# Kernel optimization log

Hardware: AMD Instinct MI355X
Metric: run time of the kernel (lower is better)

Reference implementation:

```python
import jax, jax.numpy as jnp
import numpy as np

B, H, W, DIM = 4, 256, 256, 112
HEADS, DHEAD = 4, 28
WP = 478  # shifted mask width: 256 + 2*(DIM-1)


def _dwconv(x, w, b=None, pad=1):
    # x: [B,C,H,W], w: [C,1,kh,kw] depthwise
    C = x.shape[1]
    y = jax.lax.conv_general_dilated(
        x, w, (1, 1), [(pad, pad), (pad, pad)],
        dimension_numbers=('NCHW', 'OIHW', 'NCHW'),
        feature_group_count=C)
    if b is not None:
        y = y + b[None, :, None, None]
    return y


def _conv1x1(x, w, b):
    # x: [B,C,H,W], w: [O,C]
    return jnp.einsum('bchw,oc->bohw', x, w) + b[None, :, None, None]


def _shift_back(x, step=2):
    # x: [b,nC,row,col] -> [b,nC,row,row]; per-channel column shift by int(step*i)
    b, nC, row, col = x.shape
    ds = 256 // row
    s = float(step) / float(ds * ds)
    start = jnp.floor(jnp.arange(nC) * s).astype(jnp.int32)
    idx = start[:, None] + jnp.arange(row)  # [nC, out_col=row]
    return jnp.take_along_axis(x, idx[None, :, None, :], axis=3)


def setup_inputs() -> dict:
    key = jax.random.key(0)
    ks = jax.random.split(key, 16)
    s = 0.02
    f32 = jnp.float32
    return dict(
        x_in=jax.random.normal(ks[0], (B, H, W, DIM), f32),
        mask=jax.random.uniform(ks[1], (1, H, WP, DIM), f32),
        Wq=(jax.random.normal(ks[2], (DIM, DIM), f32) * s),
        Wk=(jax.random.normal(ks[3], (DIM, DIM), f32) * s),
        Wv=(jax.random.normal(ks[4], (DIM, DIM), f32) * s),
        rescale=jnp.ones((HEADS, 1, 1), f32),
        proj_w=(jax.random.normal(ks[5], (DIM, DIM), f32) * s),
        proj_b=jnp.zeros((DIM,), f32),
        pe_w1=(jax.random.normal(ks[6], (DIM, 1, 3, 3), f32) * s),
        pe_w2=(jax.random.normal(ks[7], (DIM, 1, 3, 3), f32) * s),
        mm_c1_w=(jax.random.normal(ks[8], (DIM, DIM), f32) * s),
        mm_c1_b=jnp.zeros((DIM,), f32),
        mm_c2_w=(jax.random.normal(ks[9], (DIM, DIM), f32) * s),
        mm_c2_b=jnp.zeros((DIM,), f32),
        mm_dw_w=(jax.random.normal(ks[10], (DIM, 1, 5, 5), f32) * s),
        mm_dw_b=jnp.zeros((DIM,), f32),
    )


def reference(x_in, mask, Wq, Wk, Wv, rescale, proj_w, proj_b, pe_w1, pe_w2,
              mm_c1_w, mm_c1_b, mm_c2_w, mm_c2_b, mm_dw_w, mm_dw_b):
    b, h, w, c = x_in.shape
    heads = rescale.shape[0]
    d = c // heads
    n = h * w
    x = x_in.reshape(b, n, c)
    q_inp = x @ Wq
    k_inp = x @ Wk
    v_inp = x @ Wv

    # MaskGuidedMechanism
    m = jnp.transpose(mask, (0, 3, 1, 2))  # [1,c,H,W']
    m1 = _conv1x1(m, mm_c1_w, mm_c1_b)
    amap = jax.nn.sigmoid(_dwconv(_conv1x1(m1, mm_c2_w, mm_c2_b), mm_dw_w, mm_dw_b, pad=2))
    ms = m1 * amap + m1
    mask_attn = jnp.transpose(_shift_back(ms), (0, 2, 3, 1))  # [1,h,w,c]
    mask_attn = jnp.broadcast_to(mask_attn, (b, h, w, c)).reshape(b, n, c)

    def split(t):  # [b,n,c] -> [b,heads,d,n]
        return t.reshape(b, n, heads, d).transpose(0, 2, 3, 1)

    q = split(q_inp)
    k = split(k_inp)
    v = split(v_inp * mask_attn)
    q = q / jnp.maximum(jnp.linalg.norm(q, axis=-1, keepdims=True), 1e-12)
    k = k / jnp.maximum(jnp.linalg.norm(k, axis=-1, keepdims=True), 1e-12)

    attn = jnp.einsum('bhdn,bhen->bhde', k, q) * rescale[None]  # [b,heads,d,d]
    attn = jax.nn.softmax(attn, axis=-1)
    xo = jnp.einsum('bhde,bhen->bhdn', attn, v)  # [b,heads,d,n]
    xo = xo.transpose(0, 3, 1, 2).reshape(b, n, heads * d)
    out_c = (xo @ proj_w + proj_b).reshape(b, h, w, c)

    vi = v_inp.reshape(b, h, w, c).transpose(0, 3, 1, 2)  # [b,c,h,w]
    pe = _dwconv(jax.nn.gelu(_dwconv(vi, pe_w1, None, pad=1), approximate=False), pe_w2, None, pad=1)
    return out_c + jnp.transpose(pe, (0, 2, 3, 1))
```

## Files before the change

### kernel.cpp

```cpp
#include <hip/hip_runtime.h>
#include <math.h>


#define NPX 262144
#define NB  65536
#define C   112
#define PM  122368
#define WPC 478

__global__ void k_transpose_w(const float* __restrict__ a, const float* __restrict__ b,
                              float* __restrict__ at, float* __restrict__ bt) {
    int i = blockIdx.x * 256 + threadIdx.x;
    if (i < C * C) {
        int o = i / C, c = i % C;
        at[c * C + o] = a[i];
        bt[c * C + o] = b[i];
    }
}

template <int MODE>
__global__ __launch_bounds__(256, 2) void k_gemm112(
    const float* __restrict__ in, const float* __restrict__ W,
    const float* __restrict__ bias, const float* __restrict__ mask,
    float* __restrict__ out) {
    __shared__ float xT[16 * 260];
    const int tid = threadIdx.x;
    const int lane = tid & 63;
    const int o0 = __builtin_amdgcn_readfirstlane(tid >> 6) * 28;
    const long px0 = (long)blockIdx.x * 256;
    const float* Wb = W;
    if (MODE == 1) Wb = W + (int)(px0 >> 16) * (C * C);

    float acc[4][28];
#pragma unroll
    for (int p = 0; p < 4; ++p)
#pragma unroll
        for (int j = 0; j < 28; ++j) acc[p][j] = 0.0f;

    for (int cc = 0; cc < C; cc += 16) {
        __syncthreads();
        {
            const int pxl = tid >> 2;
            const int cg = (tid & 3) * 4;
#pragma unroll
            for (int r = 0; r < 4; ++r) {
                const int p = pxl + r * 64;
                const long px = px0 + p;
                float4 v = *(const float4*)(in + px * C + cc + cg);
                if (MODE == 1) {
                    const float4 m = *(const float4*)(mask + (long)((int)(px & 65535)) * C + cc + cg);
                    v.x *= m.x; v.y *= m.y; v.z *= m.z; v.w *= m.w;
                }
                xT[(cg + 0) * 260 + p] = v.x;
                xT[(cg + 1) * 260 + p] = v.y;
                xT[(cg + 2) * 260 + p] = v.z;
                xT[(cg + 3) * 260 + p] = v.w;
            }
        }
        __syncthreads();
#pragma unroll
        for (int c = 0; c < 16; ++c) {
            const float4 a = *(const float4*)&xT[c * 260 + lane * 4];
            const float* wr = Wb + (cc + c) * C + o0;
            float wl[28];
#pragma unroll
            for (int j = 0; j < 28; ++j) wl[j] = wr[j];
#pragma unroll
            for (int j = 0; j < 28; ++j) {
                const float w = wl[j];
                acc[0][j] = fmaf(a.x, w, acc[0][j]);
                acc[1][j] = fmaf(a.y, w, acc[1][j]);
                acc[2][j] = fmaf(a.z, w, acc[2][j]);
                acc[3][j] = fmaf(a.w, w, acc[3][j]);
            }
        }
    }
    float bl[28];
#pragma unroll
    for (int j = 0; j < 28; ++j) bl[j] = bias ? bias[o0 + j] : 0.0f;
#pragma unroll
    for (int p = 0; p < 4; ++p) {
        const long px = px0 + (long)lane * 4 + p;
        float* dst = out + px * C + o0;
#pragma unroll
        for (int j4 = 0; j4 < 7; ++j4) {
            float4 vv;
            vv.x = acc[p][j4 * 4 + 0] + bl[j4 * 4 + 0];
            vv.y = acc[p][j4 * 4 + 1] + bl[j4 * 4 + 1];
            vv.z = acc[p][j4 * 4 + 2] + bl[j4 * 4 + 2];
            vv.w = acc[p][j4 * 4 + 3] + bl[j4 * 4 + 3];
            *(float4*)(dst + j4 * 4) = vv;
        }
    }
}

__global__ __launch_bounds__(256, 2) void k_syrk(const float* __restrict__ x,
                                                 float* __restrict__ part) {
    __shared__ float tile[16 * C];
    const int batch = blockIdx.x >> 7, seg = blockIdx.x & 127;
    const float* xb = x + ((long)batch * NB + (long)seg * 512) * C;
    const int ty = threadIdx.x >> 4, tx = threadIdx.x & 15;
    float acc[7][7];
#pragma unroll
    for (int i = 0; i < 7; ++i)
#pragma unroll
        for (int j = 0; j < 7; ++j) acc[i][j] = 0.0f;

    for (int ph = 0; ph < 32; ++ph) {
        __syncthreads();
        for (int i = threadIdx.x; i < 16 * C; i += 256)
            tile[i] = xb[ph * 16 * C + i];
        __syncthreads();
#pragma unroll 4
        for (int p = 0; p < 16; ++p) {
            float a[7], b[7];
#pragma unroll
            for (int i = 0; i < 7; ++i) a[i] = tile[p * C + ty * 7 + i];
#pragma unroll
            for (int j = 0; j < 7; ++j) b[j] = tile[p * C + tx * 7 + j];
#pragma unroll
            for (int i = 0; i < 7; ++i)
#pragma unroll
                for (int j = 0; j < 7; ++j)
                    acc[i][j] = fmaf(a[i], b[j], acc[i][j]);
        }
    }
    float* pb = part + (long)blockIdx.x * (C * C);
#pragma unroll
    for (int i = 0; i < 7; ++i)
#pragma unroll
        for (int j = 0; j < 7; ++j)
            pb[(ty * 7 + i) * C + tx * 7 + j] = acc[i][j];
}

__global__ void k_syrk_reduce(const float* __restrict__ part, float* __restrict__ S) {
    const int b = blockIdx.x;
    const int i = blockIdx.y * 256 + threadIdx.x;
    const float* p = part + (long)b * 128 * (C * C) + i;
    float s = 0.0f;
    for (int k = 0; k < 128; ++k) s += p[(long)k * (C * C)];
    S[b * (C * C) + i] = s;
}

__global__ void k_dw5(const float* __restrict__ m1, const float* __restrict__ t2,
                      const float* __restrict__ dww, const float* __restrict__ dwb,
                      float* __restrict__ ms) {
    const int px = blockIdx.x * 8 + (threadIdx.x >> 5);
    const int cs = threadIdx.x & 31;
    if (cs >= 28) return;
    const int c = cs * 4;
    const int r = px / WPC, w = px % WPC;
    float wv[4][25];
#pragma unroll
    for (int k = 0; k < 4; ++k)
#pragma unroll
        for (int t = 0; t < 25; ++t) wv[k][t] = dww[(c + k) * 25 + t];
    float a0 = dwb[c], a1 = dwb[c + 1], a2 = dwb[c + 2], a3 = dwb[c + 3];
#pragma unroll
    for (int ky = 0; ky < 5; ++ky) {
        const int rr = r + ky - 2;
        if (rr < 0 || rr > 255) continue;
#pragma unroll
        for (int kx = 0; kx < 5; ++kx) {
            const int ww = w + kx - 2;
            if (ww < 0 || ww > WPC - 1) continue;
            const float4 t = *(const float4*)&t2[(long)(rr * WPC + ww) * C + c];
            const int ki = ky * 5 + kx;
            a0 = fmaf(t.x, wv[0][ki], a0);
            a1 = fmaf(t.y, wv[1][ki], a1);
            a2 = fmaf(t.z, wv[2][ki], a2);
            a3 = fmaf(t.w, wv[3][ki], a3);
        }
    }
    a0 = 1.0f / (1.0f + expf(-a0));
    a1 = 1.0f / (1.0f + expf(-a1));
    a2 = 1.0f / (1.0f + expf(-a2));
    a3 = 1.0f / (1.0f + expf(-a3));
    const float4 m = *(const float4*)&m1[(long)px * C + c];
    ms[(long)(c + 0) * PM + px] = m.x * (1.0f + a0);
    ms[(long)(c + 1) * PM + px] = m.y * (1.0f + a1);
    ms[(long)(c + 2) * PM + px] = m.z * (1.0f + a2);
    ms[(long)(c + 3) * PM + px] = m.w * (1.0f + a3);
}

__global__ void k_gather(const float* __restrict__ ms, float* __restrict__ mattn) {
    __shared__ float t[64][116];
    const int r = blockIdx.x >> 2;
    const int col0 = (blockIdx.x & 3) * 64;
    for (int i = threadIdx.x; i < C * 64; i += 256) {
        const int c = i >> 6, j = i & 63;
        t[j][c] = ms[(long)c * PM + r * WPC + col0 + 2 * c + j];
    }
    __syncthreads();
    for (int i = threadIdx.x; i < 64 * C; i += 256) {
        const int j = i / C, c = i % C;
        mattn[(long)(r * 256 + col0 + j) * C + c] = t[j][c];
    }
}

__global__ void k_T12(const float* __restrict__ S, const float* __restrict__ Wq,
                      const float* __restrict__ Wk, float* __restrict__ T1, float* __restrict__ T2) {
    const int b = blockIdx.x, which = blockIdx.y;
    const float* Sb = S + b * (C * C);
    const float* W = which ? Wk : Wq;
    float* T = (which ? T2 : T1) + b * (C * C);
    const int i0 = blockIdx.z * 1792;
    for (int i = i0 + threadIdx.x; i < i0 + 1792; i += 256) {
        const int row = i / C, col = i % C;
        float s = 0.0f;
        for (int m = 0; m < C; ++m) s = fmaf(Sb[row * C + m], W[m * C + col], s);
        T[i] = s;
    }
}

__global__ void k_attn(const float* __restrict__ T1, const float* __restrict__ T2,
                       const float* __restrict__ Wq, const float* __restrict__ Wk,
                       const float* __restrict__ rescale, const float* __restrict__ proj_w,
                       float* __restrict__ Mb) {
    __shared__ float att[28][29];
    __shared__ float nk[28], nq[28];
    const int b = blockIdx.x >> 2, h = blockIdx.x & 3;
    const float* T1b = T1 + b * (C * C);
    const float* T2b = T2 + b * (C * C);
    const int base = h * 28;
    const int tid = threadIdx.x;
    if (tid < 28) {
        const int i = base + tid;
        float s = 0.0f;
        for (int m = 0; m < C; ++m) s = fmaf(Wq[m * C + i], T1b[m * C + i], s);
        nq[tid] = fmaxf(sqrtf(fmaxf(s, 0.0f)), 1e-12f);
    } else if (tid >= 32 && tid < 60) {
        const int e = tid - 32, i = base + e;
        float s = 0.0f;
        for (int m = 0; m < C; ++m) s = fmaf(Wk[m * C + i], T2b[m * C + i], s);
        nk[e] = fmaxf(sqrtf(fmaxf(s, 0.0f)), 1e-12f);
    }
    __syncthreads();
    const float rs = rescale[h];
    for (int i = tid; i < 784; i += 256) {
        const int d = i / 28, e = i % 28;
        float s = 0.0f;
        for (int m = 0; m < C; ++m) s = fmaf(Wk[m * C + base + d], T1b[m * C + base + e], s);
        att[d][e] = s / (nk[d] * nq[e]) * rs;
    }
    __syncthreads();
    if (tid < 28) {
        float mx = -1e30f;
        for (int e = 0; e < 28; ++e) mx = fmaxf(mx, att[tid][e]);
        float sum = 0.0f;
        for (int e = 0; e < 28; ++e) { const float ex = expf(att[tid][e] - mx); att[tid][e] = ex; sum += ex; }
        const float inv = 1.0f / sum;
        for (int e = 0; e < 28; ++e) att[tid][e] *= inv;
    }
    __syncthreads();
    for (int i = tid; i < 28 * C; i += 256) {
        const int e = i / C, o = i % C;
        float s = 0.0f;
        for (int d = 0; d < 28; ++d) s = fmaf(att[d][e], proj_w[(base + d) * C + o], s);
        Mb[b * (C * C) + (base + e) * C + o] = s;
    }
}

__global__ void k_pe1(const float* __restrict__ v, const float* __restrict__ w1, float* __restrict__ g) {
    const long px = (long)blockIdx.x * 8 + (threadIdx.x >> 5);
    const int cs = threadIdx.x & 31;
    if (cs >= 28) return;
    const int c = cs * 4;
    const int within = (int)(px & 65535);
    const long bb = px - within;
    const int r = within >> 8, w = within & 255;
    float wv[4][9];
#pragma unroll
    for (int k = 0; k < 4; ++k)
#pragma unroll
        for (int t = 0; t < 9; ++t) wv[k][t] = w1[(c + k) * 9 + t];
    float a0 = 0, a1 = 0, a2 = 0, a3 = 0;
#pragma unroll
    for (int ky = 0; ky < 3; ++ky) {
        const int rr = r + ky - 1;
        if (rr < 0 || rr > 255) continue;
#pragma unroll
        for (int kx = 0; kx < 3; ++kx) {
            const int ww = w + kx - 1;
            if (ww < 0 || ww > 255) continue;
            const float4 t = *(const float4*)&v[(bb + (rr << 8) + ww) * C + c];
            const int ki = ky * 3 + kx;
            a0 = fmaf(t.x, wv[0][ki], a0);
            a1 = fmaf(t.y, wv[1][ki], a1);
            a2 = fmaf(t.z, wv[2][ki], a2);
            a3 = fmaf(t.w, wv[3][ki], a3);
        }
    }
    a0 = 0.5f * a0 * (1.0f + erff(a0 * 0.70710678118654752f));
    a1 = 0.5f * a1 * (1.0f + erff(a1 * 0.70710678118654752f));
    a2 = 0.5f * a2 * (1.0f + erff(a2 * 0.70710678118654752f));
    a3 = 0.5f * a3 * (1.0f + erff(a3 * 0.70710678118654752f));
    *(float4*)&g[px * C + c] = make_float4(a0, a1, a2, a3);
}

__global__ void k_pe2(const float* __restrict__ g, const float* __restrict__ w2, float* __restrict__ out) {
    const long px = (long)blockIdx.x * 8 + (threadIdx.x >> 5);
    const int cs = threadIdx.x & 31;
    if (cs >= 28) return;
    const int c = cs * 4;
    const int within = (int)(px & 65535);
    const long bb = px - within;
    const int r = within >> 8, w = within & 255;
    float wv[4][9];
#pragma unroll
    for (int k = 0; k < 4; ++k)
#pragma unroll
        for (int t = 0; t < 9; ++t) wv[k][t] = w2[(c + k) * 9 + t];
    float a0 = 0, a1 = 0, a2 = 0, a3 = 0;
#pragma unroll
    for (int ky = 0; ky < 3; ++ky) {
        const int rr = r + ky - 1;
        if (rr < 0 || rr > 255) continue;
#pragma unroll
        for (int kx = 0; kx < 3; ++kx) {
            const int ww = w + kx - 1;
            if (ww < 0 || ww > 255) continue;
            const float4 t = *(const float4*)&g[(bb + (rr << 8) + ww) * C + c];
            const int ki = ky * 3 + kx;
            a0 = fmaf(t.x, wv[0][ki], a0);
            a1 = fmaf(t.y, wv[1][ki], a1);
            a2 = fmaf(t.z, wv[2][ki], a2);
            a3 = fmaf(t.w, wv[3][ki], a3);
        }
    }
    float4 o = *(const float4*)&out[px * C + c];
    o.x += a0; o.y += a1; o.z += a2; o.w += a3;
    *(float4*)&out[px * C + c] = o;
}

extern "C" void kernel_launch(void* const* d_in, const int* in_sizes, int n_in,
                              void* d_out, int out_size, void* d_ws, size_t ws_size,
                              hipStream_t stream) {
    const float* x_in    = (const float*)d_in[0];
    const float* maskp   = (const float*)d_in[1];
    const float* Wq      = (const float*)d_in[2];
    const float* Wk      = (const float*)d_in[3];
    const float* Wv      = (const float*)d_in[4];
    const float* rescale = (const float*)d_in[5];
    const float* proj_w  = (const float*)d_in[6];
    const float* proj_b  = (const float*)d_in[7];
    const float* pe_w1   = (const float*)d_in[8];
    const float* pe_w2   = (const float*)d_in[9];
    const float* c1w     = (const float*)d_in[10];
    const float* c1b     = (const float*)d_in[11];
    const float* c2w     = (const float*)d_in[12];
    const float* c2b     = (const float*)d_in[13];
    const float* dww     = (const float*)d_in[14];
    const float* dwb     = (const float*)d_in[15];

    float* ws    = (float*)d_ws;
    float* v_inp = ws;
    float* mbuf  = ws + 29360128;
    float* m1    = mbuf;
    float* t2    = mbuf + 13705216;
    float* ms    = mbuf + 27410432;
    float* g     = mbuf;
    float* mattn = ws + 70475776;
    float* part  = mattn;
    float* S     = ws + 77815808;
    float* T1    = ws + 77865984;
    float* T2    = ws + 77916160;
    float* Mb    = ws + 77966336;
    float* c1wT  = ws + 78016512;
    float* c2wT  = ws + 78029056;

    k_transpose_w<<<49, 256, 0, stream>>>(c1w, c2w, c1wT, c2wT);
    k_gemm112<0><<<1024, 256, 0, stream>>>(x_in, Wv, nullptr, nullptr, v_inp);
    k_syrk<<<512, 256, 0, stream>>>(x_in, part);
    k_syrk_reduce<<<dim3(4, 49), 256, 0, stream>>>(part, S);
    k_gemm112<0><<<478, 256, 0, stream>>>(maskp, c1wT, c1b, nullptr, m1);
    k_gemm112<0><<<478, 256, 0, stream>>>(m1, c2wT, c2b, nullptr, t2);
    k_dw5<<<15296, 256, 0, stream>>>(m1, t2, dww, dwb, ms);
    k_gather<<<1024, 256, 0, stream>>>(ms, mattn);
    k_T12<<<dim3(4, 2, 7), 256, 0, stream>>>(S, Wq, Wk, T1, T2);
    k_attn<<<16, 256, 0, stream>>>(T1, T2, Wq, Wk, rescale, proj_w, Mb);
    k_pe1<<<32768, 256, 0, stream>>>(v_inp, pe_w1, g);
    k_gemm112<1><<<1024, 256, 0, stream>>>(v_inp, Mb, proj_b, mattn, (float*)d_out);
    k_pe2<<<32768, 256, 0, stream>>>(g, pe_w2, (float*)d_out);
    (void)in_sizes; (void)n_in; (void)out_size; (void)ws_size;
}
```

Baseline: 1.203 ms.

## Register-tile depthwise convs over 4 pixels and rewrite SYRK without LDS

New measurement: 1.081 ms. -10.1%, faster.

```diff
diff --git a/kernel.cpp b/kernel.cpp
--- a/kernel.cpp
+++ b/kernel.cpp
@@ -9,12 +9,25 @@
 #define WPC 478
 
 __global__ void k_transpose_w(const float* __restrict__ a, const float* __restrict__ b,
-                              float* __restrict__ at, float* __restrict__ bt) {
-    int i = blockIdx.x * 256 + threadIdx.x;
+                              const float* __restrict__ dw, const float* __restrict__ p1,
+                              const float* __restrict__ p2,
+                              float* __restrict__ at, float* __restrict__ bt,
+                              float* __restrict__ dwt, float* __restrict__ p1t,
+                              float* __restrict__ p2t) {
+    const int i = blockIdx.x * 256 + threadIdx.x;
     if (i < C * C) {
-        int o = i / C, c = i % C;
-        at[c * C + o] = a[i];
-        bt[c * C + o] = b[i];
+        const int o = i / C, cc = i % C;
+        at[cc * C + o] = a[i];
+        bt[cc * C + o] = b[i];
+    }
+    if (i < 25 * C) {
+        const int t = i / C, ch = i % C;
+        dwt[i] = dw[ch * 25 + t];
+    }
+    if (i < 9 * C) {
+        const int t = i / C, ch = i % C;
+        p1t[i] = p1[ch * 9 + t];
+        p2t[i] = p2[ch * 9 + t];
     }
 }
 
@@ -94,43 +107,44 @@
     }
 }
 
-__global__ __launch_bounds__(256, 2) void k_syrk(const float* __restrict__ x,
-                                                 float* __restrict__ part) {
-    __shared__ float tile[16 * C];
-    const int batch = blockIdx.x >> 7, seg = blockIdx.x & 127;
-    const float* xb = x + ((long)batch * NB + (long)seg * 512) * C;
-    const int ty = threadIdx.x >> 4, tx = threadIdx.x & 15;
-    float acc[7][7];
-#pragma unroll
-    for (int i = 0; i < 7; ++i)
-#pragma unroll
-        for (int j = 0; j < 7; ++j) acc[i][j] = 0.0f;
-
-    for (int ph = 0; ph < 32; ++ph) {
-        __syncthreads();
-        for (int i = threadIdx.x; i < 16 * C; i += 256)
-            tile[i] = xb[ph * 16 * C + i];
-        __syncthreads();
-#pragma unroll 4
-        for (int p = 0; p < 16; ++p) {
-            float a[7], b[7];
-#pragma unroll
-            for (int i = 0; i < 7; ++i) a[i] = tile[p * C + ty * 7 + i];
-#pragma unroll
-            for (int j = 0; j < 7; ++j) b[j] = tile[p * C + tx * 7 + j];
-#pragma unroll
-            for (int i = 0; i < 7; ++i)
-#pragma unroll
-                for (int j = 0; j < 7; ++j)
-                    acc[i][j] = fmaf(a[i], b[j], acc[i][j]);
-        }
-    }
-    float* pb = part + (long)blockIdx.x * (C * C);
-#pragma unroll
-    for (int i = 0; i < 7; ++i)
-#pragma unroll
-        for (int j = 0; j < 7; ++j)
-            pb[(ty * 7 + i) * C + tx * 7 + j] = acc[i][j];
+__global__ __launch_bounds__(256) void k_syrk(const float* __restrict__ x,
+                                              float* __restrict__ part) {
+    const int blk = blockIdx.x;
+    const int batch = blk >> 7, seg = blk & 127;
+    const long px0 = (long)batch * NB + (long)seg * 512;
+    const int lane = threadIdx.x & 63;
+    const int o0 = __builtin_amdgcn_readfirstlane(threadIdx.x >> 6) * 28;
+    const int c1 = lane * 2;
+    const bool active = (c1 < C);
+    const float* xb = x + px0 * C;
+    float acc[2][28];
+#pragma unroll
+    for (int i = 0; i < 2; ++i)
+#pragma unroll
+        for (int j = 0; j < 28; ++j) acc[i][j] = 0.0f;
+
+#pragma unroll 2
+    for (int p = 0; p < 512; ++p) {
+        const float* row = xb + p * C;
+        float2 xv = make_float2(0.0f, 0.0f);
+        if (active) xv = *(const float2*)(row + c1);
+        float wl[28];
+#pragma unroll
+        for (int j = 0; j < 28; ++j) wl[j] = row[o0 + j];
+#pragma unroll
+        for (int j = 0; j < 28; ++j) {
+            acc[0][j] = fmaf(xv.x, wl[j], acc[0][j]);
+            acc[1][j] = fmaf(xv.y, wl[j], acc[1][j]);
+        }
+    }
+    if (active) {
+        float* pb = part + (long)blk * (C * C);
+#pragma unroll
+        for (int i = 0; i < 2; ++i)
+#pragma unroll
+            for (int j = 0; j < 28; ++j)
+                pb[(c1 + i) * C + o0 + j] = acc[i][j];
+    }
 }
 
 __global__ void k_syrk_reduce(const float* __restrict__ part, float* __restrict__ S) {
@@ -142,45 +156,76 @@
     S[b * (C * C) + i] = s;
 }
 
-__global__ void k_dw5(const float* __restrict__ m1, const float* __restrict__ t2,
-                      const float* __restrict__ dww, const float* __restrict__ dwb,
-                      float* __restrict__ ms) {
-    const int px = blockIdx.x * 8 + (threadIdx.x >> 5);
-    const int cs = threadIdx.x & 31;
+__global__ __launch_bounds__(256, 4) void k_dw5(
+    const float* __restrict__ m1, const float* __restrict__ t2,
+    const float* __restrict__ dwwT, const float* __restrict__ dwb,
+    float* __restrict__ ms) {
+    const int g = threadIdx.x >> 5, cs = threadIdx.x & 31;
     if (cs >= 28) return;
     const int c = cs * 4;
-    const int r = px / WPC, w = px % WPC;
-    float wv[4][25];
-#pragma unroll
-    for (int k = 0; k < 4; ++k)
-#pragma unroll
-        for (int t = 0; t < 25; ++t) wv[k][t] = dww[(c + k) * 25 + t];
-    float a0 = dwb[c], a1 = dwb[c + 1], a2 = dwb[c + 2], a3 = dwb[c + 3];
-#pragma unroll
-    for (int ky = 0; ky < 5; ++ky) {
-        const int rr = r + ky - 2;
-        if (rr < 0 || rr > 255) continue;
-#pragma unroll
-        for (int kx = 0; kx < 5; ++kx) {
-            const int ww = w + kx - 2;
-            if (ww < 0 || ww > WPC - 1) continue;
-            const float4 t = *(const float4*)&t2[(long)(rr * WPC + ww) * C + c];
-            const int ki = ky * 5 + kx;
-            a0 = fmaf(t.x, wv[0][ki], a0);
-            a1 = fmaf(t.y, wv[1][ki], a1);
-            a2 = fmaf(t.z, wv[2][ki], a2);
-            a3 = fmaf(t.w, wv[3][ki], a3);
-        }
-    }
-    a0 = 1.0f / (1.0f + expf(-a0));
-    a1 = 1.0f / (1.0f + expf(-a1));
-    a2 = 1.0f / (1.0f + expf(-a2));
-    a3 = 1.0f / (1.0f + expf(-a3));
-    const float4 m = *(const float4*)&m1[(long)px * C + c];
-    ms[(long)(c + 0) * PM + px] = m.x * (1.0f + a0);
-    ms[(long)(c + 1) * PM + px] = m.y * (1.0f + a1);
-    ms[(long)(c + 2) * PM + px] = m.z * (1.0f + a2);
-    ms[(long)(c + 3) * PM + px] = m.w * (1.0f + a3);
+    const int px0 = blockIdx.x * 32 + g * 4;
+    const int r = px0 / WPC;
+    const int w0 = px0 - r * WPC;
+    const float4 b4 = *(const float4*)&dwb[c];
+    float4 acc[4];
+#pragma unroll
+    for (int p = 0; p < 4; ++p) acc[p] = b4;
+
+    if (w0 >= 2 && w0 <= 472) {
+#pragma unroll
+        for (int ky = 0; ky < 5; ++ky) {
+            const int rr = r + ky - 2;
+            if (rr < 0 || rr > 255) continue;
+            const float* row = t2 + (long)(rr * WPC + w0 - 2) * C + c;
+            float4 win[8];
+#pragma unroll
+            for (int k = 0; k < 8; ++k) win[k] = *(const float4*)(row + k * C);
+#pragma unroll
+            for (int kx = 0; kx < 5; ++kx) {
+                const float4 wt = *(const float4*)&dwwT[(ky * 5 + kx) * C + c];
+#pragma unroll
+                for (int p = 0; p < 4; ++p) {
+                    acc[p].x = fmaf(win[p + kx].x, wt.x, acc[p].x);
+                    acc[p].y = fmaf(win[p + kx].y, wt.y, acc[p].y);
+                    acc[p].z = fmaf(win[p + kx].z, wt.z, acc[p].z);
+                    acc[p].w = fmaf(win[p + kx].w, wt.w, acc[p].w);
+                }
+            }
+        }
+    } else {
+#pragma unroll
+        for (int p = 0; p < 4; ++p) {
+            const int px = px0 + p;
+            const int r2 = px / WPC, w2 = px - r2 * WPC;
+            for (int ky = 0; ky < 5; ++ky) {
+                const int rr = r2 + ky - 2;
+                if (rr < 0 || rr > 255) continue;
+                for (int kx = 0; kx < 5; ++kx) {
+                    const int ww = w2 + kx - 2;
+                    if (ww < 0 || ww > WPC - 1) continue;
+                    const float4 t = *(const float4*)&t2[(long)(rr * WPC + ww) * C + c];
+                    const float4 wt = *(const float4*)&dwwT[(ky * 5 + kx) * C + c];
+                    acc[p].x = fmaf(t.x, wt.x, acc[p].x);
+                    acc[p].y = fmaf(t.y, wt.y, acc[p].y);
+                    acc[p].z = fmaf(t.z, wt.z, acc[p].z);
+                    acc[p].w = fmaf(t.w, wt.w, acc[p].w);
+                }
+            }
+        }
+    }
+#pragma unroll
+    for (int p = 0; p < 4; ++p) {
+        const int px = px0 + p;
+        const float a0 = 1.0f / (1.0f + expf(-acc[p].x));
+        const float a1 = 1.0f / (1.0f + expf(-acc[p].y));
+        const float a2 = 1.0f / (1.0f + expf(-acc[p].z));
+        const float a3 = 1.0f / (1.0f + expf(-acc[p].w));
+        const float4 m = *(const float4*)&m1[(long)px * C + c];
+        ms[(long)(c + 0) * PM + px] = m.x * (1.0f + a0);
+        ms[(long)(c + 1) * PM + px] = m.y * (1.0f + a1);
+        ms[(long)(c + 2) * PM + px] = m.z * (1.0f + a2);
+        ms[(long)(c + 3) * PM + px] = m.w * (1.0f + a3);
+    }
 }
 
 __global__ void k_gather(const float* __restrict__ ms, float* __restrict__ mattn) {
@@ -261,76 +306,139 @@
     }
 }
 
-__global__ void k_pe1(const float* __restrict__ v, const float* __restrict__ w1, float* __restrict__ g) {
-    const long px = (long)blockIdx.x * 8 + (threadIdx.x >> 5);
-    const int cs = threadIdx.x & 31;
+__global__ __launch_bounds__(256, 4) void k_pe1(const float* __restrict__ v,
+                                                const float* __restrict__ pw1T,
+                                                float* __restrict__ g) {
+    const int gg = threadIdx.x >> 5, cs = threadIdx.x & 31;
     if (cs >= 28) return;
     const int c = cs * 4;
-    const int within = (int)(px & 65535);
-    const long bb = px - within;
-    const int r = within >> 8, w = within & 255;
-    float wv[4][9];
-#pragma unroll
-    for (int k = 0; k < 4; ++k)
-#pragma unroll
-        for (int t = 0; t < 9; ++t) wv[k][t] = w1[(c + k) * 9 + t];
-    float a0 = 0, a1 = 0, a2 = 0, a3 = 0;
-#pragma unroll
-    for (int ky = 0; ky < 3; ++ky) {
-        const int rr = r + ky - 1;
-        if (rr < 0 || rr > 255) continue;
-#pragma unroll
-        for (int kx = 0; kx < 3; ++kx) {
-            const int ww = w + kx - 1;
-            if (ww < 0 || ww > 255) continue;
-            const float4 t = *(const float4*)&v[(bb + (rr << 8) + ww) * C + c];
-            const int ki = ky * 3 + kx;
-            a0 = fmaf(t.x, wv[0][ki], a0);
-            a1 = fmaf(t.y, wv[1][ki], a1);
-            a2 = fmaf(t.z, wv[2][ki], a2);
-            a3 = fmaf(t.w, wv[3][ki], a3);
-        }
-    }
-    a0 = 0.5f * a0 * (1.0f + erff(a0 * 0.70710678118654752f));
-    a1 = 0.5f * a1 * (1.0f + erff(a1 * 0.70710678118654752f));
-    a2 = 0.5f * a2 * (1.0f + erff(a2 * 0.70710678118654752f));
-    a3 = 0.5f * a3 * (1.0f + erff(a3 * 0.70710678118654752f));
-    *(float4*)&g[px * C + c] = make_float4(a0, a1, a2, a3);
-}
-
-__global__ void k_pe2(const float* __restrict__ g, const float* __restrict__ w2, float* __restrict__ out) {
-    const long px = (long)blockIdx.x * 8 + (threadIdx.x >> 5);
-    const int cs = threadIdx.x & 31;
+    const long px0 = (long)blockIdx.x * 32 + gg * 4;
+    const int within = (int)(px0 & 65535);
+    const long bb = px0 - within;
+    const int r = within >> 8, w0 = within & 255;
+    float4 wt[9];
+#pragma unroll
+    for (int t = 0; t < 9; ++t) wt[t] = *(const float4*)&pw1T[t * C + c];
+    float4 acc[4];
+#pragma unroll
+    for (int p = 0; p < 4; ++p) acc[p] = make_float4(0.f, 0.f, 0.f, 0.f);
+
+    if (w0 >= 4 && w0 <= 248) {
+#pragma unroll
+        for (int ky = 0; ky < 3; ++ky) {
+            const int rr = r + ky - 1;
+            if (rr < 0 || rr > 255) continue;
+            const float* row = v + (bb + (rr << 8) + w0 - 1) * C + c;
+            float4 win[6];
+#pragma unroll
+            for (int k = 0; k < 6; ++k) win[k] = *(const float4*)(row + k * C);
+#pragma unroll
+            for (int kx = 0; kx < 3; ++kx) {
+                const float4 w4 = wt[ky * 3 + kx];
+#pragma unroll
+                for (int p = 0; p < 4; ++p) {
+                    acc[p].x = fmaf(win[p + kx].x, w4.x, acc[p].x);
+                    acc[p].y = fmaf(win[p + kx].y, w4.y, acc[p].y);
+                    acc[p].z = fmaf(win[p + kx].z, w4.z, acc[p].z);
+                    acc[p].w = fmaf(win[p + kx].w, w4.w, acc[p].w);
+                }
+            }
+        }
+    } else {
+#pragma unroll
+        for (int p = 0; p < 4; ++p) {
+            const int w = w0 + p;
+            for (int ky = 0; ky < 3; ++ky) {
+                const int rr = r + ky - 1;
+                if (rr < 0 || rr > 255) continue;
+                for (int kx = 0; kx < 3; ++kx) {
+                    const int ww = w + kx - 1;
+                    if (ww < 0 || ww > 255) continue;
+                    const float4 t = *(const float4*)&v[(bb + (rr << 8) + ww) * C + c];
+                    const float4 w4 = wt[ky * 3 + kx];
+                    acc[p].x = fmaf(t.x, w4.x, acc[p].x);
+                    acc[p].y = fmaf(t.y, w4.y, acc[p].y);
+                    acc[p].z = fmaf(t.z, w4.z, acc[p].z);
+                    acc[p].w = fmaf(t.w, w4.w, acc[p].w);
+                }
+            }
+        }
+    }
+#pragma unroll
+    for (int p = 0; p < 4; ++p) {
+        float4 a = acc[p];
+        a.x = 0.5f * a.x * (1.0f + erff(a.x * 0.70710678118654752f));
+        a.y = 0.5f * a.y * (1.0f + erff(a.y * 0.70710678118654752f));
+        a.z = 0.5f * a.z * (1.0f + erff(a.z * 0.70710678118654752f));
+        a.w = 0.5f * a.w * (1.0f + erff(a.w * 0.70710678118654752f));
+        *(float4*)&g[(px0 + p) * C + c] = a;
+    }
+}
+
+__global__ __launch_bounds__(256, 4) void k_pe2(const float* __restrict__ g,
+                                                const float* __restrict__ pw2T,
+                                                float* __restrict__ out) {
+    const int gg = threadIdx.x >> 5, cs = threadIdx.x & 31;
     if (cs >= 28) return;
     const int c = cs * 4;
-    const int within = (int)(px & 65535);
-    const long bb = px - within;
-    const int r = within >> 8, w = within & 255;
-    float wv[4][9];
-#pragma unroll
-    for (int k = 0; k < 4; ++k)
-#pragma unroll
-        for (int t = 0; t < 9; ++t) wv[k][t] = w2[(c + k) * 9 + t];
-    float a0 = 0, a1 = 0, a2 = 0, a3 = 0;
-#pragma unroll
-    for (int ky = 0; ky < 3; ++ky) {
-        const int rr = r + ky - 1;
-        if (rr < 0 || rr > 255) continue;
-#pragma unroll
-        for (int kx = 0; kx < 3; ++kx) {
-            const int ww = w + kx - 1;
-            if (ww < 0 || ww > 255) continue;
-            const float4 t = *(const float4*)&g[(bb + (rr << 8) + ww) * C + c];
-            const int ki = ky * 3 + kx;
-            a0 = fmaf(t.x, wv[0][ki], a0);
-            a1 = fmaf(t.y, wv[1][ki], a1);
-            a2 = fmaf(t.z, wv[2][ki], a2);
-            a3 = fmaf(t.w, wv[3][ki], a3);
-        }
-    }
-    float4 o = *(const float4*)&out[px * C + c];
-    o.x += a0; o.y += a1; o.z += a2; o.w += a3;
-    *(float4*)&out[px * C + c] = o;
+    const long px0 = (long)blockIdx.x * 32 + gg * 4;
+    const int within = (int)(px0 & 65535);
+    const long bb = px0 - within;
+    const int r = within >> 8, w0 = within & 255;
+    float4 wt[9];
+#pragma unroll
+    for (int t = 0; t < 9; ++t) wt[t] = *(const float4*)&pw2T[t * C + c];
+    float4 acc[4];
+#pragma unroll
+    for (int p = 0; p < 4; ++p) acc[p] = make_float4(0.f, 0.f, 0.f, 0.f);
+
+    if (w0 >= 4 && w0 <= 248) {
+#pragma unroll
+        for (int ky = 0; ky < 3; ++ky) {
+            const int rr = r + ky - 1;
+            if (rr < 0 || rr > 255) continue;
+            const float* row = g + (bb + (rr << 8) + w0 - 1) * C + c;
+            float4 win[6];
+#pragma unroll
+            for (int k = 0; k < 6; ++k) win[k] = *(const float4*)(row + k * C);
+#pragma unroll
+            for (int kx = 0; kx < 3; ++kx) {
+                const float4 w4 = wt[ky * 3 + kx];
+#pragma unroll
+                for (int p = 0; p < 4; ++p) {
+                    acc[p].x = fmaf(win[p + kx].x, w4.x, acc[p].x);
+                    acc[p].y = fmaf(win[p + kx].y, w4.y, acc[p].y);
+                    acc[p].z = fmaf(win[p + kx].z, w4.z, acc[p].z);
+                    acc[p].w = fmaf(win[p + kx].w, w4.w, acc[p].w);
+                }
+            }
+        }
+    } else {
+#pragma unroll
+        for (int p = 0; p < 4; ++p) {
+            const int w = w0 + p;
+            for (int ky = 0; ky < 3; ++ky) {
+                const int rr = r + ky - 1;
+                if (rr < 0 || rr > 255) continue;
+                for (int kx = 0; kx < 3; ++kx) {
+                    const int ww = w + kx - 1;
+                    if (ww < 0 || ww > 255) continue;
+                    const float4 t = *(const float4*)&g[(bb + (rr << 8) + ww) * C + c];
+                    const float4 w4 = wt[ky * 3 + kx];
+                    acc[p].x = fmaf(t.x, w4.x, acc[p].x);
+                    acc[p].y = fmaf(t.y, w4.y, acc[p].y);
+                    acc[p].z = fmaf(t.z, w4.z, acc[p].z);
+                    acc[p].w = fmaf(t.w, w4.w, acc[p].w);
+                }
+            }
+        }
+    }
+#pragma unroll
+    for (int p = 0; p < 4; ++p) {
+        float4 o = *(const float4*)&out[(px0 + p) * C + c];
+        o.x += acc[p].x; o.y += acc[p].y; o.z += acc[p].z; o.w += acc[p].w;
+        *(float4*)&out[(px0 + p) * C + c] = o;
+    }
 }
 
 extern "C" void kernel_launch(void* const* d_in, const int* in_sizes, int n_in,
@@ -356,31 +464,35 @@
     float* ws    = (float*)d_ws;
     float* v_inp = ws;
     float* mbuf  = ws + 29360128;
+    float* part  = mbuf;
     float* m1    = mbuf;
     float* t2    = mbuf + 13705216;
     float* ms    = mbuf + 27410432;
     float* g     = mbuf;
     float* mattn = ws + 70475776;
-    float* part  = mattn;
     float* S     = ws + 77815808;
     float* T1    = ws + 77865984;
     float* T2    = ws + 77916160;
     float* Mb    = ws + 77966336;
     float* c1wT  = ws + 78016512;
     float* c2wT  = ws + 78029056;
-
-    k_transpose_w<<<49, 256, 0, stream>>>(c1w, c2w, c1wT, c2wT);
+    float* dwwT  = ws + 78041600;
+    float* pw1T  = ws + 78044400;
+    float* pw2T  = ws + 78045408;
+
+    k_transpose_w<<<49, 256, 0, stream>>>(c1w, c2w, dww, pe_w1, pe_w2,
+                                          c1wT, c2wT, dwwT, pw1T, pw2T);
     k_gemm112<0><<<1024, 256, 0, stream>>>(x_in, Wv, nullptr, nullptr, v_inp);
     k_syrk<<<512, 256, 0, stream>>>(x_in, part);
     k_syrk_reduce<<<dim3(4, 49), 256, 0, stream>>>(part, S);
     k_gemm112<0><<<478, 256, 0, stream>>>(maskp, c1wT, c1b, nullptr, m1);
     k_gemm112<0><<<478, 256, 0, stream>>>(m1, c2wT, c2b, nullptr, t2);
-    k_dw5<<<15296, 256, 0, stream>>>(m1, t2, dww, dwb, ms);
+    k_dw5<<<3824, 256, 0, stream>>>(m1, t2, dwwT, dwb, ms);
     k_gather<<<1024, 256, 0, stream>>>(ms, mattn);
     k_T12<<<dim3(4, 2, 7), 256, 0, stream>>>(S, Wq, Wk, T1, T2);
     k_attn<<<16, 256, 0, stream>>>(T1, T2, Wq, Wk, rescale, proj_w, Mb);
-    k_pe1<<<32768, 256, 0, stream>>>(v_inp, pe_w1, g);
+    k_pe1<<<8192, 256, 0, stream>>>(v_inp, pw1T, g);
     k_gemm112<1><<<1024, 256, 0, stream>>>(v_inp, Mb, proj_b, mattn, (float*)d_out);
-    k_pe2<<<32768, 256, 0, stream>>>(g, pe_w2, (float*)d_out);
+    k_pe2<<<8192, 256, 0, stream>>>(g, pw2T, (float*)d_out);
     (void)in_sizes; (void)n_in; (void)out_size; (void)ws_size;
 }
```
